# Kernel optimization log

Measured on AMD Instinct MI355X. Metric: run time of the kernel, lower is better.

## Reference

```python
import jax, jax.numpy as jnp
import numpy as np

B, S, ENC, DEC, ATTN = 32, 4096, 512, 512, 512


def setup_inputs() -> dict:
    key = jax.random.key(0)
    k1, k2, k3, k4, k5, k6 = jax.random.split(key, 6)
    h = jax.random.normal(k1, (B, DEC), dtype=jnp.float32)
    enc_out = jax.random.normal(k2, (B, S, ENC), dtype=jnp.float32)
    mask = jax.random.randint(k3, (B, S), 0, 2).astype(bool)
    # torch nn.Linear(in, out, bias=False): y = x @ W.T with W [out, in].
    # Store weights as [in, out] so y = x @ W; same math.
    sc = 1.0 / np.sqrt(DEC)
    W_h = jax.random.normal(k4, (DEC, ATTN), dtype=jnp.float32) * sc
    W_s = jax.random.normal(k5, (ENC, ATTN), dtype=jnp.float32) * sc
    v = jax.random.normal(k6, (ATTN,), dtype=jnp.float32) * sc
    return {"h": h, "enc_out": enc_out, "mask": mask, "W_h": W_h, "W_s": W_s, "v": v}


def reference(h, enc_out, mask, W_h, W_s, v):
    # query: [B, 1, A]; key: [B, S, A]
    query = (h @ W_h)[:, None, :]
    key = jnp.einsum("bse,ea->bsa", enc_out, W_s)
    energy = jnp.tanh(query + key)                    # [B, S, A]
    score = jnp.einsum("bsa,a->bs", energy, v)        # v^T tanh(...)
    score = jnp.where(mask, jnp.float32(-1e9), score)
    attn = jax.nn.softmax(score, axis=-1)             # [B, S]
    ctx = jnp.einsum("bs,bse->be", attn, enc_out)     # weighted sum
    return (ctx, attn)
```

## Files before the change

kernel.cpp:

```cpp
#include <hip/hip_runtime.h>
#include <hip/hip_bf16.h>
#include <math.h>

#define BB 32
#define SS 4096
#define EE 512
#define AA 512

typedef short bf16x8 __attribute__((ext_vector_type(8)));
typedef float f32x4 __attribute__((ext_vector_type(4)));
typedef unsigned short u16x4 __attribute__((ext_vector_type(4)));

__device__ __forceinline__ unsigned short f2bf(float f) {
  unsigned int u = __float_as_uint(f);
  u += 0x7fffu + ((u >> 16) & 1u);
  return (unsigned short)(u >> 16);
}

__device__ __forceinline__ float bf2f(unsigned short s) {
  return __uint_as_float(((unsigned int)s) << 16);
}

__device__ __forceinline__ float tanh_fast(float x) {
  return 1.f - 2.f / (__expf(2.f * x) + 1.f);
}

__global__ void query_kernel(const float* __restrict__ h,
                             const float* __restrict__ Wh,
                             float* __restrict__ q) {
  __shared__ float hrow[EE];
  int b = blockIdx.x;
  int t = threadIdx.x;
  for (int i = t; i < EE; i += 256) hrow[i] = h[b * EE + i];
  __syncthreads();
  float a0 = 0.f, a1 = 0.f;
  for (int e = 0; e < EE; ++e) {
    float hv = hrow[e];
    a0 += hv * Wh[e * AA + t];
    a1 += hv * Wh[e * AA + t + 256];
  }
  q[b * AA + t] = a0;
  q[b * AA + t + 256] = a1;
}

__global__ void wst_kernel(const float* __restrict__ Ws,
                           unsigned short* __restrict__ Wst) {
  __shared__ unsigned short tile[64][65];
  const int a0 = blockIdx.x * 64, e0 = blockIdx.y * 64;
  const int t = threadIdx.x;
  const int c = t & 63, r0 = t >> 6;
#pragma unroll
  for (int i = 0; i < 16; ++i) {
    int e = r0 + i * 4;
    tile[c][e] = f2bf(Ws[(size_t)(e0 + e) * AA + a0 + c]);
  }
  __syncthreads();
#pragma unroll
  for (int i = 0; i < 16; ++i) {
    int a = r0 + i * 4;
    Wst[(size_t)(a0 + a) * EE + e0 + c] = tile[a][c];
  }
}

__global__ __launch_bounds__(512, 4) void fused_kernel(
    const float* __restrict__ enc, const unsigned short* __restrict__ Wst,
    const float* __restrict__ q, const float* __restrict__ v,
    const int* __restrict__ mask,
    float* __restrict__ rawscore,
    float* __restrict__ ctxp,
    float* __restrict__ mbuf) {
  __shared__ __align__(16) unsigned short Atile[64 * 512];
  __shared__ float spart[8][64];
  __shared__ float wrow[64];
  const int b = blockIdx.y, chunk = blockIdx.x;
  const int s0 = chunk * 64;
  const int tid = threadIdx.x;
  const int w = tid >> 6, lane = tid & 63;
  const int quad = lane >> 4, l16 = lane & 15;
  const int n0 = w * 64;

  const int rbase = tid >> 4;
  const int c4 = tid & 15;
  const int sw3 = (rbase & 7) << 3;
  const float4* src4 = (const float4*)(enc + ((size_t)b * SS + s0) * EE);
  const float4* g0 = src4 + rbase * 128 + c4;
  const float4* g1 = g0 + 32 * 128;
  unsigned short* st0 = &Atile[rbase * 512 + ((c4 * 4) ^ sw3)];
  unsigned short* st1 = st0 + 32 * 512;

  const unsigned short* wb = Wst + (size_t)(n0 + l16) * EE + quad * 8;

  f32x4 acc[4][4];
#pragma unroll
  for (int m = 0; m < 4; ++m)
#pragma unroll
    for (int j = 0; j < 4; ++j) acc[m][j] = (f32x4){0.f, 0.f, 0.f, 0.f};

  float4 rb[2][2];
  rb[0][0] = g0[0];
  rb[0][1] = g1[0];

#pragma unroll
  for (int c = 0; c < 8; ++c) {
    const int cur = c & 1, nxt = cur ^ 1;
    {
      float4 x = rb[cur][0];
      u16x4 p;
      p.x = f2bf(x.x); p.y = f2bf(x.y); p.z = f2bf(x.z); p.w = f2bf(x.w);
      *(u16x4*)(st0 + c * 64) = p;
      float4 y = rb[cur][1];
      u16x4 p2;
      p2.x = f2bf(y.x); p2.y = f2bf(y.y); p2.z = f2bf(y.z); p2.w = f2bf(y.w);
      *(u16x4*)(st1 + c * 64) = p2;
    }
    if (c < 7) {
      rb[nxt][0] = g0[(c + 1) * 16];
      rb[nxt][1] = g1[(c + 1) * 16];
    }
    asm volatile("s_waitcnt lgkmcnt(0)" ::: "memory");
    __builtin_amdgcn_s_barrier();
#pragma unroll
    for (int kk = 0; kk < 2; ++kk) {
      const int k0 = c * 64 + kk * 32;
      bf16x8 aF[4];
#pragma unroll
      for (int m = 0; m < 4; ++m) {
        const int row = m * 16 + l16;
        aF[m] = *(const bf16x8*)&Atile[row * 512 +
                                       ((k0 + quad * 8) ^ ((row & 7) << 3))];
      }
#pragma unroll
      for (int j = 0; j < 4; ++j) {
        bf16x8 bF = *(const bf16x8*)&wb[(size_t)j * 16 * EE + k0];
#pragma unroll
        for (int m = 0; m < 4; ++m)
          acc[m][j] = __builtin_amdgcn_mfma_f32_16x16x32_bf16(aF[m], bF,
                                                              acc[m][j], 0, 0, 0);
      }
    }
  }

  float srow[4][4];
#pragma unroll
  for (int m = 0; m < 4; ++m)
#pragma unroll
    for (int r = 0; r < 4; ++r) srow[m][r] = 0.f;
#pragma unroll
  for (int j = 0; j < 4; ++j) {
    float qn = q[b * AA + n0 + j * 16 + l16];
    float vn = v[n0 + j * 16 + l16];
#pragma unroll
    for (int m = 0; m < 4; ++m)
#pragma unroll
      for (int r = 0; r < 4; ++r)
        srow[m][r] += tanh_fast(qn + acc[m][j][r]) * vn;
  }
#pragma unroll
  for (int m = 0; m < 4; ++m)
#pragma unroll
    for (int r = 0; r < 4; ++r) {
      float s = srow[m][r];
      s += __shfl_xor(s, 1, 64);
      s += __shfl_xor(s, 2, 64);
      s += __shfl_xor(s, 4, 64);
      s += __shfl_xor(s, 8, 64);
      if (l16 == 0) spart[w][m * 16 + quad * 4 + r] = s;
    }
  __syncthreads();

  if (tid < 64) {
    float raw = 0.f;
#pragma unroll
    for (int ww = 0; ww < 8; ++ww) raw += spart[ww][tid];
    float sc = mask[(size_t)b * SS + s0 + tid] ? -1e9f : raw;
    rawscore[(size_t)b * SS + s0 + tid] = sc;
    float mx = sc;
    for (int off = 1; off < 64; off <<= 1)
      mx = fmaxf(mx, __shfl_xor(mx, off, 64));
    wrow[tid] = __expf(sc - mx);
    if (tid == 0) mbuf[b * 64 + chunk] = mx;
  }
  __syncthreads();

  {
    const int e = tid;
    float a = 0.f;
#pragma unroll 8
    for (int row = 0; row < 64; ++row)
      a += wrow[row] * bf2f(Atile[row * 512 + (e ^ ((row & 7) << 3))]);
    ctxp[((size_t)b * 64 + chunk) * EE + e] = a;
  }
}

__global__ __launch_bounds__(512) void finalize_kernel(
    float* __restrict__ attn, const float* __restrict__ ctxp,
    const float* __restrict__ mbuf, float* __restrict__ ctx) {
  __shared__ float red[16];
  __shared__ float fc[64];
  int b = blockIdx.x, t = threadIdx.x;
  float* row = attn + (size_t)b * SS;
  float vals[8];
  float m = -3e38f;
#pragma unroll
  for (int i = 0; i < 8; ++i) {
    float x = row[i * 512 + t];
    vals[i] = x;
    m = fmaxf(m, x);
  }
  for (int off = 1; off < 64; off <<= 1) m = fmaxf(m, __shfl_xor(m, off, 64));
  int wv = t >> 6, ln = t & 63;
  if (ln == 0) red[wv] = m;
  __syncthreads();
  m = red[0];
#pragma unroll
  for (int i = 1; i < 8; ++i) m = fmaxf(m, red[i]);
  float sum = 0.f;
#pragma unroll
  for (int i = 0; i < 8; ++i) { vals[i] = __expf(vals[i] - m); sum += vals[i]; }
  for (int off = 1; off < 64; off <<= 1) sum += __shfl_xor(sum, off, 64);
  if (ln == 0) red[8 + wv] = sum;
  __syncthreads();
  sum = 0.f;
#pragma unroll
  for (int i = 0; i < 8; ++i) sum += red[8 + i];
  float inv = 1.f / sum;
#pragma unroll
  for (int i = 0; i < 8; ++i) row[i * 512 + t] = vals[i] * inv;

  if (t < 64) fc[t] = __expf(mbuf[b * 64 + t] - m) * inv;
  __syncthreads();
  {
    const float* p = ctxp + (size_t)b * 64 * EE + t;
    float s = 0.f;
#pragma unroll
    for (int c = 0; c < 64; ++c) s += fc[c] * p[c * EE];
    ctx[b * EE + t] = s;
  }
}

extern "C" void kernel_launch(void* const* d_in, const int* in_sizes, int n_in,
                              void* d_out, int out_size, void* d_ws, size_t ws_size,
                              hipStream_t stream) {
  const float* h    = (const float*)d_in[0];
  const float* enc  = (const float*)d_in[1];
  const int*   mask = (const int*)d_in[2];
  const float* Wh   = (const float*)d_in[3];
  const float* Ws   = (const float*)d_in[4];
  const float* v    = (const float*)d_in[5];

  float* out  = (float*)d_out;
  float* ctx  = out;
  float* attn = out + BB * EE;

  char* ws = (char*)d_ws;
  float* qws = (float*)ws;                         ws += (size_t)BB * AA * 4;
  unsigned short* Wst = (unsigned short*)ws;       ws += (size_t)AA * EE * 2;
  float* ctxp = (float*)ws;                        ws += (size_t)BB * 64 * EE * 4;
  float* mbuf = (float*)ws;

  hipLaunchKernelGGL(query_kernel, dim3(32), dim3(256), 0, stream, h, Wh, qws);
  hipLaunchKernelGGL(wst_kernel, dim3(8, 8), dim3(256), 0, stream, Ws, Wst);
  hipLaunchKernelGGL(fused_kernel, dim3(SS / 64, BB), dim3(512), 0, stream,
                     enc, Wst, qws, v, mask, attn, ctxp, mbuf);
  hipLaunchKernelGGL(finalize_kernel, dim3(BB), dim3(512), 0, stream,
                     attn, ctxp, mbuf, ctx);
}
```

Before: 529.9 us.

## Pre-convert encoder outputs to bf16 in a merged prep kernel

Merges the query and weight-transpose kernels into one prep kernel, which also converts the whole enc_out tensor (256 MB fp32) to a bf16 workspace copy when the workspace is large enough. The fused kernel then loads bf16 rows directly into LDS instead of converting fp32 on the fly. The aim is to cut the fused kernel's global reads and its conversion work. The cost is an extra full pass that reads fp32 enc_out and writes the bf16 copy, so total memory traffic goes up.

```diff
diff --git a/kernel.cpp b/kernel.cpp
--- a/kernel.cpp
+++ b/kernel.cpp
@@ -25,50 +25,66 @@
   return 1.f - 2.f / (__expf(2.f * x) + 1.f);
 }
 
-__global__ void query_kernel(const float* __restrict__ h,
-                             const float* __restrict__ Wh,
-                             float* __restrict__ q) {
-  __shared__ float hrow[EE];
-  int b = blockIdx.x;
-  int t = threadIdx.x;
-  for (int i = t; i < EE; i += 256) hrow[i] = h[b * EE + i];
-  __syncthreads();
-  float a0 = 0.f, a1 = 0.f;
-  for (int e = 0; e < EE; ++e) {
-    float hv = hrow[e];
-    a0 += hv * Wh[e * AA + t];
-    a1 += hv * Wh[e * AA + t + 256];
-  }
-  q[b * AA + t] = a0;
-  q[b * AA + t + 256] = a1;
-}
-
-__global__ void wst_kernel(const float* __restrict__ Ws,
-                           unsigned short* __restrict__ Wst) {
-  __shared__ unsigned short tile[64][65];
-  const int a0 = blockIdx.x * 64, e0 = blockIdx.y * 64;
+__global__ __launch_bounds__(512) void prep_kernel(
+    const float* __restrict__ h, const float* __restrict__ Wh,
+    const float* __restrict__ Ws, const float* __restrict__ enc,
+    float* __restrict__ q, unsigned short* __restrict__ Wst,
+    unsigned short* __restrict__ encb, int do_conv) {
+  __shared__ __align__(16) unsigned char plds[64 * 65 * 2];
+  const int blk = blockIdx.x;
   const int t = threadIdx.x;
-  const int c = t & 63, r0 = t >> 6;
-#pragma unroll
-  for (int i = 0; i < 16; ++i) {
-    int e = r0 + i * 4;
-    tile[c][e] = f2bf(Ws[(size_t)(e0 + e) * AA + a0 + c]);
-  }
-  __syncthreads();
-#pragma unroll
-  for (int i = 0; i < 16; ++i) {
-    int a = r0 + i * 4;
-    Wst[(size_t)(a0 + a) * EE + e0 + c] = tile[a][c];
+  if (blk < 32) {
+    float* hrow = (float*)plds;
+    const int b = blk;
+    hrow[t] = h[b * EE + t];
+    __syncthreads();
+    float a = 0.f;
+#pragma unroll 8
+    for (int e = 0; e < EE; ++e) a += hrow[e] * Wh[e * AA + t];
+    q[b * AA + t] = a;
+  } else if (blk < 96) {
+    unsigned short(*tile)[65] = (unsigned short(*)[65])plds;
+    const int idx = blk - 32;
+    const int a0 = (idx & 7) * 64, e0 = (idx >> 3) * 64;
+    const int c = t & 63, r = t >> 6;
+#pragma unroll
+    for (int i = 0; i < 8; ++i) {
+      int e = r + i * 8;
+      tile[c][e] = f2bf(Ws[(size_t)(e0 + e) * AA + a0 + c]);
+    }
+    __syncthreads();
+#pragma unroll
+    for (int i = 0; i < 8; ++i) {
+      int a = r + i * 8;
+      Wst[(size_t)(a0 + a) * EE + e0 + c] = tile[a][c];
+    }
+  } else if (do_conv) {
+    const size_t ci = (size_t)(blk - 96);
+    const float4* s4 = (const float4*)enc;
+    bf16x8* d8 = (bf16x8*)encb;
+#pragma unroll
+    for (int it = 0; it < 8; ++it) {
+      size_t g = ci * 4096 + (size_t)it * 512 + t;
+      float4 x = s4[g * 2];
+      float4 y = s4[g * 2 + 1];
+      bf16x8 vv;
+      vv[0] = (short)f2bf(x.x); vv[1] = (short)f2bf(x.y);
+      vv[2] = (short)f2bf(x.z); vv[3] = (short)f2bf(x.w);
+      vv[4] = (short)f2bf(y.x); vv[5] = (short)f2bf(y.y);
+      vv[6] = (short)f2bf(y.z); vv[7] = (short)f2bf(y.w);
+      d8[g] = vv;
+    }
   }
 }
 
 __global__ __launch_bounds__(512, 4) void fused_kernel(
-    const float* __restrict__ enc, const unsigned short* __restrict__ Wst,
-    const float* __restrict__ q, const float* __restrict__ v,
-    const int* __restrict__ mask,
+    const float* __restrict__ enc, const unsigned short* __restrict__ encb,
+    const unsigned short* __restrict__ Wst, const float* __restrict__ q,
+    const float* __restrict__ v, const int* __restrict__ mask,
     float* __restrict__ rawscore,
     float* __restrict__ ctxp,
-    float* __restrict__ mbuf) {
+    float* __restrict__ mbuf,
+    int use_bf) {
   __shared__ __align__(16) unsigned short Atile[64 * 512];
   __shared__ float spart[8][64];
   __shared__ float wrow[64];
@@ -79,6 +95,11 @@
   const int quad = lane >> 4, l16 = lane & 15;
   const int n0 = w * 64;
 
+  const int brow = tid >> 3, bpiece = tid & 7;
+  const bf16x8* gB =
+      (const bf16x8*)(encb + ((size_t)b * SS + s0 + brow) * EE) + bpiece;
+  unsigned short* stB_row = &Atile[brow * 512];
+
   const int rbase = tid >> 4;
   const int c4 = tid & 15;
   const int sw3 = (rbase & 7) << 3;
@@ -96,14 +117,21 @@
 #pragma unroll
     for (int j = 0; j < 4; ++j) acc[m][j] = (f32x4){0.f, 0.f, 0.f, 0.f};
 
+  bf16x8 rbB[3];
   float4 rb[2][2];
-  rb[0][0] = g0[0];
-  rb[0][1] = g1[0];
+  if (use_bf) {
+    rbB[0] = gB[0]; rbB[1] = gB[8]; rbB[2] = gB[16];
+  } else {
+    rb[0][0] = g0[0]; rb[0][1] = g1[0];
+  }
 
 #pragma unroll
   for (int c = 0; c < 8; ++c) {
-    const int cur = c & 1, nxt = cur ^ 1;
-    {
+    if (use_bf) {
+      *(bf16x8*)&stB_row[(((c * 8 + bpiece) ^ (brow & 7)) * 8)] = rbB[c % 3];
+      if (c + 3 < 8) rbB[(c + 3) % 3] = gB[(c + 3) * 8];
+    } else {
+      const int cur = c & 1;
       float4 x = rb[cur][0];
       u16x4 p;
       p.x = f2bf(x.x); p.y = f2bf(x.y); p.z = f2bf(x.z); p.w = f2bf(x.w);
@@ -112,10 +140,10 @@
       u16x4 p2;
       p2.x = f2bf(y.x); p2.y = f2bf(y.y); p2.z = f2bf(y.z); p2.w = f2bf(y.w);
       *(u16x4*)(st1 + c * 64) = p2;
-    }
-    if (c < 7) {
-      rb[nxt][0] = g0[(c + 1) * 16];
-      rb[nxt][1] = g1[(c + 1) * 16];
+      if (c + 1 < 8) {
+        rb[cur ^ 1][0] = g0[(c + 1) * 16];
+        rb[cur ^ 1][1] = g1[(c + 1) * 16];
+      }
     }
     asm volatile("s_waitcnt lgkmcnt(0)" ::: "memory");
     __builtin_amdgcn_s_barrier();
@@ -253,15 +281,19 @@
   float* attn = out + BB * EE;
 
   char* ws = (char*)d_ws;
-  float* qws = (float*)ws;                         ws += (size_t)BB * AA * 4;
-  unsigned short* Wst = (unsigned short*)ws;       ws += (size_t)AA * EE * 2;
-  float* ctxp = (float*)ws;                        ws += (size_t)BB * 64 * EE * 4;
-  float* mbuf = (float*)ws;
-
-  hipLaunchKernelGGL(query_kernel, dim3(32), dim3(256), 0, stream, h, Wh, qws);
-  hipLaunchKernelGGL(wst_kernel, dim3(8, 8), dim3(256), 0, stream, Ws, Wst);
+  float* qws = (float*)ws;                   ws += (size_t)BB * AA * 4;
+  unsigned short* Wst = (unsigned short*)ws; ws += (size_t)AA * EE * 2;
+  float* ctxp = (float*)ws;                  ws += (size_t)BB * 64 * EE * 4;
+  float* mbuf = (float*)ws;                  ws += (size_t)BB * 64 * 4;
+  unsigned short* encb = (unsigned short*)ws;
+
+  const size_t need = (size_t)(ws - (char*)d_ws) + (size_t)BB * SS * EE * 2;
+  const int use_bf = (d_ws != nullptr && ws_size >= need) ? 1 : 0;
+
+  hipLaunchKernelGGL(prep_kernel, dim3(use_bf ? 2144 : 96), dim3(512), 0, stream,
+                     h, Wh, Ws, enc, qws, Wst, encb, use_bf);
   hipLaunchKernelGGL(fused_kernel, dim3(SS / 64, BB), dim3(512), 0, stream,
-                     enc, Wst, qws, v, mask, attn, ctxp, mbuf);
+                     enc, encb, Wst, qws, v, mask, attn, ctxp, mbuf, use_bf);
   hipLaunchKernelGGL(finalize_kernel, dim3(BB), dim3(512), 0, stream,
                      attn, ctxp, mbuf, ctx);
 }
```

Result: slower. 601.8 us (+13.6%).

## Merge prep kernels, pre-swizzle W_s into MFMA fragment layout, split query GEMV

Applied to the files above, without the earlier changes.

Replaces the separate query and W_s transpose kernels with one 288-block prep kernel. Query computation is split over 8 e-slices per batch into partial sums, which the fused kernel now adds up. W_s is converted to bf16 and stored in the exact per-lane MFMA B-fragment order, so each B-fragment load in the main loop is a contiguous 16-byte-per-lane read. This removes a launch and the strided B loads, at the cost of eight extra q loads per output column and a prep kernel whose Ws reads are strided.

```diff
diff --git a/kernel.cpp b/kernel.cpp
--- a/kernel.cpp
+++ b/kernel.cpp
@@ -25,46 +25,41 @@
   return 1.f - 2.f / (__expf(2.f * x) + 1.f);
 }
 
-__global__ void query_kernel(const float* __restrict__ h,
-                             const float* __restrict__ Wh,
-                             float* __restrict__ q) {
-  __shared__ float hrow[EE];
-  int b = blockIdx.x;
-  int t = threadIdx.x;
-  for (int i = t; i < EE; i += 256) hrow[i] = h[b * EE + i];
-  __syncthreads();
-  float a0 = 0.f, a1 = 0.f;
-  for (int e = 0; e < EE; ++e) {
-    float hv = hrow[e];
-    a0 += hv * Wh[e * AA + t];
-    a1 += hv * Wh[e * AA + t + 256];
-  }
-  q[b * AA + t] = a0;
-  q[b * AA + t + 256] = a1;
-}
-
-__global__ void wst_kernel(const float* __restrict__ Ws,
-                           unsigned short* __restrict__ Wst) {
-  __shared__ unsigned short tile[64][65];
-  const int a0 = blockIdx.x * 64, e0 = blockIdx.y * 64;
+__global__ __launch_bounds__(512) void prep_kernel(
+    const float* __restrict__ h, const float* __restrict__ Wh,
+    const float* __restrict__ Ws, float* __restrict__ qpart,
+    unsigned short* __restrict__ WF) {
+  __shared__ float hrow[64];
+  const int blk = blockIdx.x;
   const int t = threadIdx.x;
-  const int c = t & 63, r0 = t >> 6;
-#pragma unroll
-  for (int i = 0; i < 16; ++i) {
-    int e = r0 + i * 4;
-    tile[c][e] = f2bf(Ws[(size_t)(e0 + e) * AA + a0 + c]);
-  }
-  __syncthreads();
-#pragma unroll
-  for (int i = 0; i < 16; ++i) {
-    int a = r0 + i * 4;
-    Wst[(size_t)(a0 + a) * EE + e0 + c] = tile[a][c];
+  if (blk < 256) {
+    const int b = blk >> 3, sl = blk & 7, e0 = sl * 64;
+    if (t < 64) hrow[t] = h[b * EE + e0 + t];
+    __syncthreads();
+    float a = 0.f;
+#pragma unroll 8
+    for (int e = 0; e < 64; ++e) a += hrow[e] * Wh[(size_t)(e0 + e) * AA + t];
+    qpart[(size_t)blk * AA + t] = a;
+  } else {
+    const int nb = blk - 256;
+#pragma unroll
+    for (int rep = 0; rep < 2; ++rep) {
+      const int idx = rep * 512 + t;
+      const int kb = idx >> 6, lane = idx & 63;
+      const int krow = kb * 32 + ((lane >> 4) << 3);
+      const int acol = nb * 16 + (lane & 15);
+      bf16x8 vv;
+#pragma unroll
+      for (int i = 0; i < 8; ++i)
+        vv[i] = (short)f2bf(Ws[(size_t)(krow + i) * AA + acol]);
+      ((bf16x8*)WF)[(size_t)nb * 1024 + idx] = vv;
+    }
   }
 }
 
 __global__ __launch_bounds__(512, 4) void fused_kernel(
-    const float* __restrict__ enc, const unsigned short* __restrict__ Wst,
-    const float* __restrict__ q, const float* __restrict__ v,
+    const float* __restrict__ enc, const unsigned short* __restrict__ WF,
+    const float* __restrict__ qpart, const float* __restrict__ v,
     const int* __restrict__ mask,
     float* __restrict__ rawscore,
     float* __restrict__ ctxp,
@@ -88,7 +83,7 @@
   unsigned short* st0 = &Atile[rbase * 512 + ((c4 * 4) ^ sw3)];
   unsigned short* st1 = st0 + 32 * 512;
 
-  const unsigned short* wb = Wst + (size_t)(n0 + l16) * EE + quad * 8;
+  const bf16x8* wfl = (const bf16x8*)WF + lane;
 
   f32x4 acc[4][4];
 #pragma unroll
@@ -97,12 +92,11 @@
     for (int j = 0; j < 4; ++j) acc[m][j] = (f32x4){0.f, 0.f, 0.f, 0.f};
 
   float4 rb[2][2];
-  rb[0][0] = g0[0];
-  rb[0][1] = g1[0];
+  rb[0][0] = g0[0]; rb[0][1] = g1[0];
 
 #pragma unroll
   for (int c = 0; c < 8; ++c) {
-    const int cur = c & 1, nxt = cur ^ 1;
+    const int cur = c & 1;
     {
       float4 x = rb[cur][0];
       u16x4 p;
@@ -113,9 +107,9 @@
       p2.x = f2bf(y.x); p2.y = f2bf(y.y); p2.z = f2bf(y.z); p2.w = f2bf(y.w);
       *(u16x4*)(st1 + c * 64) = p2;
     }
-    if (c < 7) {
-      rb[nxt][0] = g0[(c + 1) * 16];
-      rb[nxt][1] = g1[(c + 1) * 16];
+    if (c + 1 < 8) {
+      rb[cur ^ 1][0] = g0[(c + 1) * 16];
+      rb[cur ^ 1][1] = g1[(c + 1) * 16];
     }
     asm volatile("s_waitcnt lgkmcnt(0)" ::: "memory");
     __builtin_amdgcn_s_barrier();
@@ -131,7 +125,7 @@
       }
 #pragma unroll
       for (int j = 0; j < 4; ++j) {
-        bf16x8 bF = *(const bf16x8*)&wb[(size_t)j * 16 * EE + k0];
+        bf16x8 bF = wfl[(size_t)(((w * 4 + j) * 16 + c * 2 + kk) * 64)];
 #pragma unroll
         for (int m = 0; m < 4; ++m)
           acc[m][j] = __builtin_amdgcn_mfma_f32_16x16x32_bf16(aF[m], bF,
@@ -147,7 +141,10 @@
     for (int r = 0; r < 4; ++r) srow[m][r] = 0.f;
 #pragma unroll
   for (int j = 0; j < 4; ++j) {
-    float qn = q[b * AA + n0 + j * 16 + l16];
+    const float* qp = qpart + (size_t)b * 8 * AA + n0 + j * 16 + l16;
+    float qn = 0.f;
+#pragma unroll
+    for (int sl = 0; sl < 8; ++sl) qn += qp[sl * AA];
     float vn = v[n0 + j * 16 + l16];
 #pragma unroll
     for (int m = 0; m < 4; ++m)
@@ -253,15 +250,15 @@
   float* attn = out + BB * EE;
 
   char* ws = (char*)d_ws;
-  float* qws = (float*)ws;                         ws += (size_t)BB * AA * 4;
-  unsigned short* Wst = (unsigned short*)ws;       ws += (size_t)AA * EE * 2;
-  float* ctxp = (float*)ws;                        ws += (size_t)BB * 64 * EE * 4;
+  float* qpart = (float*)ws;                 ws += (size_t)BB * 8 * AA * 4;
+  unsigned short* WF = (unsigned short*)ws;  ws += (size_t)AA * EE * 2;
+  float* ctxp = (float*)ws;                  ws += (size_t)BB * 64 * EE * 4;
   float* mbuf = (float*)ws;
 
-  hipLaunchKernelGGL(query_kernel, dim3(32), dim3(256), 0, stream, h, Wh, qws);
-  hipLaunchKernelGGL(wst_kernel, dim3(8, 8), dim3(256), 0, stream, Ws, Wst);
+  hipLaunchKernelGGL(prep_kernel, dim3(288), dim3(512), 0, stream,
+                     h, Wh, Ws, qpart, WF);
   hipLaunchKernelGGL(fused_kernel, dim3(SS / 64, BB), dim3(512), 0, stream,
-                     enc, Wst, qws, v, mask, attn, ctxp, mbuf);
+                     enc, WF, qpart, v, mask, attn, ctxp, mbuf);
   hipLaunchKernelGGL(finalize_kernel, dim3(BB), dim3(512), 0, stream,
                      attn, ctxp, mbuf, ctx);
 }
```

Measured after the change: 520.9 us. Within noise of the previous version (-1.7%).
